# Kernel tuning notes

Hardware: AMD Instinct MI355X
Metric: run time of the kernel (lower is better)

The kernel has to match this reference:

```python
import jax, jax.numpy as jnp
import numpy as np
from jax import lax

NUM_HEADS = 16
DIM = 1024
BATCH = 4
SEQ = 2048


def setup_inputs() -> dict:
    key = jax.random.key(0)
    ks = jax.random.split(key, 12)
    f32 = jnp.float32
    q = jax.random.normal(ks[0], (BATCH, SEQ, DIM), dtype=f32)
    k = jax.random.normal(ks[1], (BATCH, SEQ, DIM), dtype=f32)
    v = jax.random.normal(ks[2], (BATCH, SEQ, DIM), dtype=f32)
    lim = 1.0 / np.sqrt(DIM)  # nn.Linear default init range
    Wi = jax.random.uniform(ks[3], (DIM, DIM), minval=-lim, maxval=lim, dtype=f32)
    bi = jax.random.uniform(ks[4], (DIM,), minval=-lim, maxval=lim, dtype=f32)
    Wg = jax.random.uniform(ks[5], (DIM, DIM), minval=-lim, maxval=lim, dtype=f32)
    bg = jax.random.uniform(ks[6], (DIM,), minval=-lim, maxval=lim, dtype=f32)
    Wo = jax.random.uniform(ks[7], (DIM, DIM), minval=-lim, maxval=lim, dtype=f32)
    bo = jax.random.uniform(ks[8], (DIM,), minval=-lim, maxval=lim, dtype=f32)
    A = jax.random.normal(ks[9], (DIM, DIM), dtype=f32) * 0.1
    Bm = jax.random.normal(ks[10], (DIM, DIM), dtype=f32) * 0.1
    decay = jnp.full((1, NUM_HEADS, 1), 0.9, dtype=f32)
    return dict(q=q, k=k, v=v, Wi=Wi, bi=bi, Wg=Wg, bg=bg, A=A, Bm=Bm,
                Wo=Wo, bo=bo, decay=decay)


def reference(q, k, v, Wi, bi, Wg, bg, A, Bm, Wo, bo, decay):
    B, S, D = q.shape
    H = decay.shape[1]
    hd = D // H
    # time-major heads: [S, B, H, hd]
    qh = jnp.moveaxis(q.reshape(B, S, H, hd), 1, 0)
    kh = jnp.moveaxis(k.reshape(B, S, H, hd), 1, 0)
    vh = jnp.moveaxis(v.reshape(B, S, H, hd), 1, 0)

    def step(carry, xs):
        r, state = carry
        qt, kt, vt = xs
        r = decay * r + kt * vt                         # [B, H, hd]
        retained = (qt * r).reshape(B, D)               # [B, D]
        inp = retained @ Wi.T + bi
        gate = jax.nn.sigmoid(inp @ Wg.T + bg)
        blended = gate * state + (1.0 - gate) * inp
        state = jnp.tanh(blended @ A.T + inp @ Bm.T)
        out = state @ Wo.T + bo                         # [B, D]
        return (r, state), out

    r0 = jnp.zeros((B, H, hd), dtype=q.dtype)
    s0 = jnp.zeros((B, D), dtype=q.dtype)
    _, outs = lax.scan(step, (r0, s0), (qh, kh, vh))     # outs: [S, B, D]
    return jnp.moveaxis(outs, 0, 1)                      # [B, S, D]
```

## Files before the change

kernel.cpp:

```cpp
#include <hip/hip_runtime.h>
#include <hip/hip_bf16.h>
#include <math.h>

#define BATCH 4
#define SEQ   2048
#define DIM   1024
#define MROWS (SEQ*BATCH)
#define BIGN  ((size_t)MROWS*DIM)

typedef float v2f __attribute__((ext_vector_type(2)));

__global__ __launch_bounds__(256) void scan_a(const float* __restrict__ K,
    const float* __restrict__ V, const float* __restrict__ dec_p,
    float* __restrict__ E)
{
  int id  = blockIdx.x*256 + threadIdx.x;
  int c   = id >> 12;
  int rem = id & 4095;
  int b   = rem >> 10;
  int dc  = rem & 1023;
  float dec = dec_p[dc >> 6];
  size_t base = ((size_t)b*SEQ + (size_t)c*32)*DIM + dc;
  float r = 0.f;
  #pragma unroll 4
  for (int i = 0; i < 32; ++i) {
    float kv = K[base + (size_t)i*DIM] * V[base + (size_t)i*DIM];
    r = fmaf(dec, r, kv);
  }
  E[(size_t)c*4096 + rem] = r;
}

__global__ __launch_bounds__(256) void scan_b(const float* __restrict__ E,
    const float* __restrict__ dec_p, float* __restrict__ carry)
{
  int id = blockIdx.x*256 + threadIdx.x;
  int dc = id & 1023;
  float dec = dec_p[dc >> 6];
  float d2 = dec*dec, d4 = d2*d2, d8 = d4*d4, d16 = d8*d8, d32 = d16*d16;
  float r = 0.f;
  #pragma unroll 1
  for (int c = 0; c < 64; ++c) {
    carry[(size_t)c*4096 + id] = r;
    r = fmaf(d32, r, E[(size_t)c*4096 + id]);
  }
}

__global__ __launch_bounds__(256) void scan_c(const float* __restrict__ Q,
    const float* __restrict__ K, const float* __restrict__ V,
    const float* __restrict__ dec_p, const float* __restrict__ carry,
    float* __restrict__ ret)
{
  int id  = blockIdx.x*256 + threadIdx.x;
  int c   = id >> 12;
  int rem = id & 4095;
  int b   = rem >> 10;
  int dc  = rem & 1023;
  float dec = dec_p[dc >> 6];
  size_t base = ((size_t)b*SEQ + (size_t)c*32)*DIM + dc;
  float r = carry[(size_t)c*4096 + rem];
  #pragma unroll 1
  for (int i = 0; i < 32; ++i) {
    int t = c*32 + i;
    float kv = K[base + (size_t)i*DIM] * V[base + (size_t)i*DIM];
    r = fmaf(dec, r, kv);
    ret[((size_t)t*BATCH + b)*DIM + dc] = Q[base + (size_t)i*DIM] * r;
  }
}

#define GM 128
#define GN 128
#define GK 16
#define LDG 132

template<int MODE>
__global__ __launch_bounds__(256) void gemm_k(
    const float* __restrict__ X, const float* __restrict__ W,
    const float* __restrict__ bias, float* __restrict__ C,
    const float* __restrict__ inp, float* __restrict__ u_out,
    float* __restrict__ outf)
{
  __shared__ float Xs[GK][LDG];
  __shared__ float Ws[GK][LDG];
  const int tid = threadIdx.x;
  const int m0 = blockIdx.y * GM;
  const int n0 = blockIdx.x * GN;
  const int tx = tid & 15, ty = tid >> 4;
  v2f acc[8][4] = {};
  #pragma unroll 1
  for (int kb = 0; kb < DIM; kb += GK) {
    #pragma unroll
    for (int h = 0; h < 2; ++h) {
      int idx = tid + h*256;
      int r   = idx >> 2;
      int kc  = (idx & 3) << 2;
      float4 xv = *(const float4*)(X + (size_t)(m0+r)*DIM + kb + kc);
      Xs[kc+0][r] = xv.x; Xs[kc+1][r] = xv.y;
      Xs[kc+2][r] = xv.z; Xs[kc+3][r] = xv.w;
      float4 wv2 = *(const float4*)(W + (size_t)(n0+r)*DIM + kb + kc);
      Ws[kc+0][r] = wv2.x; Ws[kc+1][r] = wv2.y;
      Ws[kc+2][r] = wv2.z; Ws[kc+3][r] = wv2.w;
    }
    __syncthreads();
    #pragma unroll
    for (int kk = 0; kk < GK; ++kk) {
      float4 a0 = *(const float4*)&Xs[kk][ty*8];
      float4 a1 = *(const float4*)&Xs[kk][ty*8 + 4];
      float4 w0 = *(const float4*)&Ws[kk][tx*4];
      float4 w1 = *(const float4*)&Ws[kk][64 + tx*4];
      v2f wv[4] = {{w0.x,w0.y},{w0.z,w0.w},{w1.x,w1.y},{w1.z,w1.w}};
      float av[8] = {a0.x,a0.y,a0.z,a0.w,a1.x,a1.y,a1.z,a1.w};
      #pragma unroll
      for (int i = 0; i < 8; ++i) {
        v2f ab = {av[i], av[i]};
        #pragma unroll
        for (int j = 0; j < 4; ++j)
          acc[i][j] = __builtin_elementwise_fma(ab, wv[j], acc[i][j]);
      }
    }
    __syncthreads();
  }
  float bj[8];
  #pragma unroll
  for (int j = 0; j < 8; ++j) {
    int n = n0 + ((j < 4) ? (tx*4 + j) : (64 + tx*4 + (j - 4)));
    bj[j] = (MODE == 0 || MODE == 1 || MODE == 3) ? bias[n] : 0.f;
  }
  #pragma unroll
  for (int i = 0; i < 8; ++i) {
    int m = m0 + ty*8 + i;
    #pragma unroll
    for (int j = 0; j < 8; ++j) {
      int n = n0 + ((j < 4) ? (tx*4 + j) : (64 + tx*4 + (j - 4)));
      size_t off = (size_t)m*DIM + n;
      float vv = acc[i][j >> 1][j & 1] + bj[j];
      if (MODE == 2) vv += C[off];
      if (MODE == 1) {
        float gv = 1.f/(1.f + expf(-vv));
        C[off] = gv;
        u_out[off] = (1.f - gv) * inp[off];
      } else if (MODE == 3) {
        outf[((size_t)(m & 3)*SEQ + (size_t)(m >> 2))*DIM + n] = vv;
      } else {
        C[off] = vv;
      }
    }
  }
}

#define RBLK 64

__global__ __launch_bounds__(512, 2) void recur_k(
    const float* __restrict__ A, const float* __restrict__ g,
    const float* __restrict__ dpre, float* __restrict__ s,
    unsigned long long* __restrict__ sf)
{
  __shared__ __align__(16) float xs[2][8*132 + 4];
  const int tid = threadIdx.x;
  const int w   = tid >> 6;
  const int ln  = tid & 63;
  const int b   = blockIdx.x >> 4;
  const int blk = blockIdx.x & 15;
  const int row = blk*64 + w*8 + (ln >> 3);
  const int ks  = ln & 7;

  const size_t slotstride = (size_t)BATCH*512;
  unsigned long long* sfb = sf + (size_t)b*512;

  float4 areg[32];
  #pragma unroll
  for (int j = 0; j < 32; ++j)
    areg[j] = *(const float4*)(A + (size_t)row*DIM + ks*128 + 4*j);
  const v2f* a2 = reinterpret_cast<const v2f*>(areg);

  const int xoff = (tid >> 6)*132 + ((2*tid) & 127);

  float2 gvc = *(const float2*)(g + (size_t)b*DIM + 2*tid);
  float  dvc = (ks == 0) ? dpre[(size_t)b*DIM + row] : 0.f;
  unsigned long long sampA = 0, sampB = 0;

  #pragma unroll 1
  for (int t = 0; t < SEQ; ++t) {
    const int buf = t & 1;
    v2f acc0 = {0.f,0.f}, acc1 = {0.f,0.f}, acc2 = {0.f,0.f}, acc3 = {0.f,0.f};
    if (t > 0) {
      const unsigned wl = ((unsigned)(t + 1) >> 1) & 1u;
      unsigned long long* pw =
          sfb + (size_t)((t - 1) & 1)*slotstride + tid;
      union { unsigned long long u; float f[2]; } wv;
      if ((unsigned)(sampA & 1u) == wl)       wv.u = sampA;
      else if ((unsigned)(sampB & 1u) == wl)  wv.u = sampB;
      else {
        int guard = 0;
        for (;;) {
          unsigned long long x0 = __hip_atomic_load(pw, __ATOMIC_RELAXED,
                                                    __HIP_MEMORY_SCOPE_AGENT);
          unsigned long long x1 = __hip_atomic_load(pw, __ATOMIC_RELAXED,
                                                    __HIP_MEMORY_SCOPE_AGENT);
          if ((unsigned)(x0 & 1u) == wl) { wv.u = x0; break; }
          if ((unsigned)(x1 & 1u) == wl) { wv.u = x1; break; }
          if (++guard > (1 << 22))       { wv.u = x1; break; }
        }
      }

      *(float2*)(xs[buf] + xoff) = make_float2(gvc.x * wv.f[0],
                                               gvc.y * wv.f[1]);
      asm volatile("s_waitcnt lgkmcnt(0)\n\ts_barrier" ::: "memory");

      const float* xb = xs[buf] + ks*132;
      #pragma unroll
      for (int j = 0; j < 32; j += 4) {
        float4 x0 = *(const float4*)(xb + 4*j);
        float4 x1 = *(const float4*)(xb + 4*j + 4);
        float4 x2 = *(const float4*)(xb + 4*j + 8);
        float4 x3 = *(const float4*)(xb + 4*j + 12);
        v2f x0l = {x0.x, x0.y}, x0h = {x0.z, x0.w};
        v2f x1l = {x1.x, x1.y}, x1h = {x1.z, x1.w};
        v2f x2l = {x2.x, x2.y}, x2h = {x2.z, x2.w};
        v2f x3l = {x3.x, x3.y}, x3h = {x3.z, x3.w};
        acc0 = __builtin_elementwise_fma(a2[2*j+0], x0l, acc0);
        acc0 = __builtin_elementwise_fma(a2[2*j+1], x0h, acc0);
        acc1 = __builtin_elementwise_fma(a2[2*j+2], x1l, acc1);
        acc1 = __builtin_elementwise_fma(a2[2*j+3], x1h, acc1);
        acc2 = __builtin_elementwise_fma(a2[2*j+4], x2l, acc2);
        acc2 = __builtin_elementwise_fma(a2[2*j+5], x2h, acc2);
        acc3 = __builtin_elementwise_fma(a2[2*j+6], x3l, acc3);
        acc3 = __builtin_elementwise_fma(a2[2*j+7], x3h, acc3);
      }
    }
    v2f accp = (acc0 + acc1) + (acc2 + acc3);
    float sum = accp.x + accp.y;
    sum += __shfl_xor(sum, 1, 64);
    sum += __shfl_xor(sum, 2, 64);
    sum += __shfl_xor(sum, 4, 64);
    float val = 0.f;
    if (ks == 0) {
      float zz  = sum + dvc;
      float e2x = __builtin_amdgcn_exp2f(zz * 2.8853900817779268f);
      val = 1.0f - 2.0f * __builtin_amdgcn_rcpf(e2x + 1.0f);
    }
    float pv = __shfl_xor(val, 8, 64);
    const unsigned tg = ((unsigned)(t + 2) >> 1) & 1u;
    if ((ln & 15) == 0) {
      union { unsigned long long u; unsigned ui[2]; } pk;
      pk.ui[0] = (__float_as_uint(val) & ~1u) | tg;
      pk.ui[1] = (__float_as_uint(pv)  & ~1u) | tg;
      __hip_atomic_store(sfb + (size_t)(t & 1)*slotstride + (row >> 1), pk.u,
                         __ATOMIC_RELAXED, __HIP_MEMORY_SCOPE_AGENT);
    }
    if (ks == 0)
      s[((size_t)t*4 + b)*DIM + row] = val;

    if (t + 1 < SEQ) {
      gvc = *(const float2*)(g + ((size_t)(t + 1)*4 + b)*DIM + 2*tid);
      dvc = (ks == 0) ? dpre[((size_t)(t + 1)*4 + b)*DIM + row] : 0.f;
      unsigned long long* pw1 = sfb + (size_t)(t & 1)*slotstride + tid;
      sampA = __hip_atomic_load(pw1, __ATOMIC_RELAXED,
                                __HIP_MEMORY_SCOPE_AGENT);
      sampB = __hip_atomic_load(pw1, __ATOMIC_RELAXED,
                                __HIP_MEMORY_SCOPE_AGENT);
      asm volatile("" ::: "memory");
    }
  }
}

extern "C" void kernel_launch(void* const* d_in, const int* in_sizes, int n_in,
                              void* d_out, int out_size, void* d_ws, size_t ws_size,
                              hipStream_t stream)
{
  (void)in_sizes; (void)n_in; (void)out_size;
  const float* q   = (const float*)d_in[0];
  const float* k   = (const float*)d_in[1];
  const float* v   = (const float*)d_in[2];
  const float* Wi  = (const float*)d_in[3];
  const float* bi  = (const float*)d_in[4];
  const float* Wg  = (const float*)d_in[5];
  const float* bg  = (const float*)d_in[6];
  const float* A   = (const float*)d_in[7];
  const float* Bm  = (const float*)d_in[8];
  const float* Wo  = (const float*)d_in[9];
  const float* bo  = (const float*)d_in[10];
  const float* dec = (const float*)d_in[11];

  const size_t sf_bytes = (size_t)2*BATCH*512*sizeof(unsigned long long);
  size_t need = (4*BIGN + 2*(size_t)64*4096)*sizeof(float) + sf_bytes;
  if (ws_size < need) return;

  float* b0 = (float*)d_ws;
  float* b1 = b0 + BIGN;
  float* b2 = b1 + BIGN;
  float* b3 = b2 + BIGN;
  float* E     = b3 + BIGN;
  float* carry = E + (size_t)64*4096;
  unsigned long long* sf = (unsigned long long*)(carry + (size_t)64*4096);
  float* outp  = (float*)d_out;

  hipMemsetAsync(sf, 0, sf_bytes, stream);

  scan_a<<<1024, 256, 0, stream>>>(k, v, dec, E);
  scan_b<<<16,   256, 0, stream>>>(E, dec, carry);
  scan_c<<<1024, 256, 0, stream>>>(q, k, v, dec, carry, b0);

  dim3 gg(DIM/GN, MROWS/GM);
  gemm_k<0><<<gg, 256, 0, stream>>>(b0, Wi, bi, b1, nullptr, nullptr, nullptr);
  gemm_k<1><<<gg, 256, 0, stream>>>(b1, Wg, bg, b2, b1, b0, nullptr);
  gemm_k<4><<<gg, 256, 0, stream>>>(b0, A,  nullptr, b3, nullptr, nullptr, nullptr);
  gemm_k<2><<<gg, 256, 0, stream>>>(b1, Bm, nullptr, b3, nullptr, nullptr, nullptr);

  recur_k<<<RBLK, 512, 0, stream>>>(A, b2, b3, b0, sf);

  gemm_k<3><<<gg, 256, 0, stream>>>(b0, Wo, bo, nullptr, nullptr, nullptr, outp);
}
```

Measured before the change: 5.892 ms.

## Spread recurrent matvec over more blocks with 32-lane row dot products

The sequential tanh recurrence kernel is re-partitioned from 16 blocks per batch (64 rows each, 8 lanes per row holding 128 weights) to 64 blocks per batch (16 rows each, 32 lanes per row holding 32 weights). This cuts per-step FMA work and register pressure per thread, and puts more CUs on the per-timestep critical path. It also swaps the double-buffered padded LDS tile for a single XOR-swizzled buffer plus an extra barrier. It drops the speculative early sampling of the flag slots. In exchange, four times as many blocks take part in the global flag exchange each step, and the early sample no longer hides polling latency.

Measured after the change: 7.184 ms. +21.9%, slower.

```diff
diff --git a/kernel.cpp b/kernel.cpp
--- a/kernel.cpp
+++ b/kernel.cpp
@@ -147,119 +147,99 @@
   }
 }
 
-#define RBLK 64
+#define RBLK 256
 
 __global__ __launch_bounds__(512, 2) void recur_k(
     const float* __restrict__ A, const float* __restrict__ g,
     const float* __restrict__ dpre, float* __restrict__ s,
     unsigned long long* __restrict__ sf)
 {
-  __shared__ __align__(16) float xs[2][8*132 + 4];
+  __shared__ __align__(16) float xs[1024 + 8];
   const int tid = threadIdx.x;
   const int w   = tid >> 6;
   const int ln  = tid & 63;
-  const int b   = blockIdx.x >> 4;
-  const int blk = blockIdx.x & 15;
-  const int row = blk*64 + w*8 + (ln >> 3);
-  const int ks  = ln & 7;
+  const int h   = ln >> 5;
+  const int l5  = ln & 31;
+  const int b   = blockIdx.x >> 6;
+  const int blk = blockIdx.x & 63;
+  const int row = blk*16 + w*2 + h;
 
   const size_t slotstride = (size_t)BATCH*512;
   unsigned long long* sfb = sf + (size_t)b*512;
 
-  float4 areg[32];
-  #pragma unroll
-  for (int j = 0; j < 32; ++j)
-    areg[j] = *(const float4*)(A + (size_t)row*DIM + ks*128 + 4*j);
-  const v2f* a2 = reinterpret_cast<const v2f*>(areg);
-
-  const int xoff = (tid >> 6)*132 + ((2*tid) & 127);
+  float4 atmp[8];
+  #pragma unroll
+  for (int j = 0; j < 8; ++j)
+    atmp[j] = *(const float4*)(A + (size_t)row*DIM + l5*32 + 4*j);
+  v2f a2[16];
+  #pragma unroll
+  for (int j = 0; j < 8; ++j) {
+    a2[2*j]   = (v2f){atmp[j].x, atmp[j].y};
+    a2[2*j+1] = (v2f){atmp[j].z, atmp[j].w};
+  }
+
+  const int m15   = l5 & 15;
+  const int wphys = (tid >> 4)*32 + (((tid & 15) ^ ((tid >> 4) & 15)) << 1);
+  int roff[16];
+  #pragma unroll
+  for (int j2 = 0; j2 < 16; ++j2)
+    roff[j2] = l5*32 + ((j2 ^ m15) << 1);
 
   float2 gvc = *(const float2*)(g + (size_t)b*DIM + 2*tid);
-  float  dvc = (ks == 0) ? dpre[(size_t)b*DIM + row] : 0.f;
-  unsigned long long sampA = 0, sampB = 0;
+  float  dvc = dpre[(size_t)b*DIM + row];
 
   #pragma unroll 1
   for (int t = 0; t < SEQ; ++t) {
-    const int buf = t & 1;
-    v2f acc0 = {0.f,0.f}, acc1 = {0.f,0.f}, acc2 = {0.f,0.f}, acc3 = {0.f,0.f};
+    v2f acc = {0.f, 0.f};
     if (t > 0) {
       const unsigned wl = ((unsigned)(t + 1) >> 1) & 1u;
-      unsigned long long* pw =
-          sfb + (size_t)((t - 1) & 1)*slotstride + tid;
+      unsigned long long* pw = sfb + (size_t)((t - 1) & 1)*slotstride + tid;
       union { unsigned long long u; float f[2]; } wv;
-      if ((unsigned)(sampA & 1u) == wl)       wv.u = sampA;
-      else if ((unsigned)(sampB & 1u) == wl)  wv.u = sampB;
-      else {
-        int guard = 0;
-        for (;;) {
-          unsigned long long x0 = __hip_atomic_load(pw, __ATOMIC_RELAXED,
-                                                    __HIP_MEMORY_SCOPE_AGENT);
-          unsigned long long x1 = __hip_atomic_load(pw, __ATOMIC_RELAXED,
-                                                    __HIP_MEMORY_SCOPE_AGENT);
-          if ((unsigned)(x0 & 1u) == wl) { wv.u = x0; break; }
-          if ((unsigned)(x1 & 1u) == wl) { wv.u = x1; break; }
-          if (++guard > (1 << 22))       { wv.u = x1; break; }
-        }
-      }
-
-      *(float2*)(xs[buf] + xoff) = make_float2(gvc.x * wv.f[0],
-                                               gvc.y * wv.f[1]);
+      int guard = 0;
+      for (;;) {
+        unsigned long long x0 = __hip_atomic_load(pw, __ATOMIC_RELAXED,
+                                                  __HIP_MEMORY_SCOPE_AGENT);
+        unsigned long long x1 = __hip_atomic_load(pw, __ATOMIC_RELAXED,
+                                                  __HIP_MEMORY_SCOPE_AGENT);
+        if ((unsigned)(x0 & 1u) == wl) { wv.u = x0; break; }
+        if ((unsigned)(x1 & 1u) == wl) { wv.u = x1; break; }
+        if (++guard > (1 << 22))       { wv.u = x1; break; }
+      }
+
+      *(float2*)(xs + wphys) = make_float2(gvc.x * wv.f[0], gvc.y * wv.f[1]);
       asm volatile("s_waitcnt lgkmcnt(0)\n\ts_barrier" ::: "memory");
 
-      const float* xb = xs[buf] + ks*132;
       #pragma unroll
-      for (int j = 0; j < 32; j += 4) {
-        float4 x0 = *(const float4*)(xb + 4*j);
-        float4 x1 = *(const float4*)(xb + 4*j + 4);
-        float4 x2 = *(const float4*)(xb + 4*j + 8);
-        float4 x3 = *(const float4*)(xb + 4*j + 12);
-        v2f x0l = {x0.x, x0.y}, x0h = {x0.z, x0.w};
-        v2f x1l = {x1.x, x1.y}, x1h = {x1.z, x1.w};
-        v2f x2l = {x2.x, x2.y}, x2h = {x2.z, x2.w};
-        v2f x3l = {x3.x, x3.y}, x3h = {x3.z, x3.w};
-        acc0 = __builtin_elementwise_fma(a2[2*j+0], x0l, acc0);
-        acc0 = __builtin_elementwise_fma(a2[2*j+1], x0h, acc0);
-        acc1 = __builtin_elementwise_fma(a2[2*j+2], x1l, acc1);
-        acc1 = __builtin_elementwise_fma(a2[2*j+3], x1h, acc1);
-        acc2 = __builtin_elementwise_fma(a2[2*j+4], x2l, acc2);
-        acc2 = __builtin_elementwise_fma(a2[2*j+5], x2h, acc2);
-        acc3 = __builtin_elementwise_fma(a2[2*j+6], x3l, acc3);
-        acc3 = __builtin_elementwise_fma(a2[2*j+7], x3h, acc3);
-      }
-    }
-    v2f accp = (acc0 + acc1) + (acc2 + acc3);
-    float sum = accp.x + accp.y;
+      for (int j2 = 0; j2 < 16; ++j2) {
+        v2f xv = *(const v2f*)(xs + roff[j2]);
+        acc = __builtin_elementwise_fma(a2[j2], xv, acc);
+      }
+    }
+    float sum = acc.x + acc.y;
     sum += __shfl_xor(sum, 1, 64);
     sum += __shfl_xor(sum, 2, 64);
     sum += __shfl_xor(sum, 4, 64);
-    float val = 0.f;
-    if (ks == 0) {
-      float zz  = sum + dvc;
-      float e2x = __builtin_amdgcn_exp2f(zz * 2.8853900817779268f);
-      val = 1.0f - 2.0f * __builtin_amdgcn_rcpf(e2x + 1.0f);
-    }
-    float pv = __shfl_xor(val, 8, 64);
+    sum += __shfl_xor(sum, 8, 64);
+    sum += __shfl_xor(sum, 16, 64);
+    float zz  = sum + dvc;
+    float e2x = __builtin_amdgcn_exp2f(zz * 2.8853900817779268f);
+    float val = 1.0f - 2.0f * __builtin_amdgcn_rcpf(e2x + 1.0f);
+    float pv = __shfl_xor(val, 32, 64);
     const unsigned tg = ((unsigned)(t + 2) >> 1) & 1u;
-    if ((ln & 15) == 0) {
+    if (ln == 0) {
       union { unsigned long long u; unsigned ui[2]; } pk;
       pk.ui[0] = (__float_as_uint(val) & ~1u) | tg;
       pk.ui[1] = (__float_as_uint(pv)  & ~1u) | tg;
-      __hip_atomic_store(sfb + (size_t)(t & 1)*slotstride + (row >> 1), pk.u,
+      __hip_atomic_store(sfb + (size_t)(t & 1)*slotstride + (blk*8 + w), pk.u,
                          __ATOMIC_RELAXED, __HIP_MEMORY_SCOPE_AGENT);
-    }
-    if (ks == 0)
-      s[((size_t)t*4 + b)*DIM + row] = val;
-
+      *(float2*)(s + ((size_t)t*4 + b)*DIM + blk*16 + w*2)
+          = make_float2(val, pv);
+    }
     if (t + 1 < SEQ) {
       gvc = *(const float2*)(g + ((size_t)(t + 1)*4 + b)*DIM + 2*tid);
-      dvc = (ks == 0) ? dpre[((size_t)(t + 1)*4 + b)*DIM + row] : 0.f;
-      unsigned long long* pw1 = sfb + (size_t)(t & 1)*slotstride + tid;
-      sampA = __hip_atomic_load(pw1, __ATOMIC_RELAXED,
-                                __HIP_MEMORY_SCOPE_AGENT);
-      sampB = __hip_atomic_load(pw1, __ATOMIC_RELAXED,
-                                __HIP_MEMORY_SCOPE_AGENT);
-      asm volatile("" ::: "memory");
-    }
+      dvc = dpre[((size_t)(t + 1)*4 + b)*DIM + row];
+    }
+    asm volatile("s_barrier" ::: "memory");
   }
 }
 
```
